# Kernel tuning notes

Hardware: AMD Instinct MI355X
Metric: run time of the kernel (lower is better)

## Reference

```python
import jax, jax.numpy as jnp
import numpy as np

B, S, D, H = 4, 2048, 1024, 16
HD = D // H


def setup_inputs() -> dict:
    key = jax.random.key(0)
    ks = jax.random.split(key, 12)
    s = 1.0 / np.sqrt(D)
    return {
        "query": jax.random.normal(ks[0], (B, S, D), jnp.float32),
        "key_": jax.random.normal(ks[1], (B, S, D), jnp.float32),
        "value": jax.random.normal(ks[2], (B, S, D), jnp.float32),
        "mask": jnp.ones((1, 1, S, S), dtype=bool),
        "Wq": jax.random.normal(ks[3], (D, D), jnp.float32) * s,
        "bq": jnp.zeros((D,), jnp.float32),
        "Wk": jax.random.normal(ks[4], (D, D), jnp.float32) * s,
        "bk": jnp.zeros((D,), jnp.float32),
        "Wv": jax.random.normal(ks[5], (D, D), jnp.float32) * s,
        "bv": jnp.zeros((D,), jnp.float32),
        "Wo": jax.random.normal(ks[6], (D, D), jnp.float32) * s,
        "bo": jnp.zeros((D,), jnp.float32),
    }


def reference(query, key_, value, mask, Wq, bq, Wk, bk, Wv, bv, Wo, bo):
    # Linear projections (torch Linear: x @ W^T + b; here W stored as (in, out))
    Q = query @ Wq + bq   # [B,S,D]
    K = key_ @ Wk + bk
    V = value @ Wv + bv
    # split heads -> [B,H,S,HD]
    Q = Q.reshape(B, S, H, HD).transpose(0, 2, 1, 3)
    K = K.reshape(B, S, H, HD).transpose(0, 2, 1, 3)
    V = V.reshape(B, S, H, HD).transpose(0, 2, 1, 3)
    scores = jnp.einsum("bhqd,bhkd->bhqk", Q, K) / jnp.sqrt(jnp.float32(HD))
    scores = jnp.where(mask, scores, jnp.float32(-jnp.inf))
    attn = jax.nn.softmax(scores, axis=-1)          # [B,H,S,S]
    ctx = jnp.einsum("bhqk,bhkd->bhqd", attn, V)    # dropout = identity (eval)
    ctx = ctx.transpose(0, 2, 1, 3).reshape(B, S, D)
    out = ctx @ Wo + bo
    return out, attn
```

## Files before the change

### kernel.cpp

```cpp
#include <hip/hip_runtime.h>
#include <hip/hip_bf16.h>

typedef __attribute__((ext_vector_type(4))) unsigned short u16x4;
typedef __attribute__((ext_vector_type(8))) short short8;
typedef __attribute__((ext_vector_type(4))) short short4b;
typedef __attribute__((ext_vector_type(4))) float f32x4;

__device__ inline unsigned short f2bf(float f) {
    union { float f; unsigned int i; } v; v.f = f;
    unsigned int r = v.i + 0x7fffu + ((v.i >> 16) & 1u);
    return (unsigned short)(r >> 16);
}

__device__ inline unsigned int pk_bf16(float a, float b) {
    union { __hip_bfloat162 h; unsigned int u; } cv;
    cv.h = __float22bfloat162_rn(float2{a, b});
    return cv.u;
}

#define MFMA_PV(a, b, c) __builtin_amdgcn_mfma_f32_16x16x16bf16_1k((a), (b), (c), 0, 0, 0)
#define MFMA32(a, b, c) __builtin_amdgcn_mfma_f32_16x16x32_bf16((a), (b), (c), 0, 0, 0)

#define SCL 0.18033688011112042f

__device__ inline void gload_lds16(const unsigned short* g, unsigned short* l) {
    __builtin_amdgcn_global_load_lds(
        (const __attribute__((address_space(1))) void*)g,
        (__attribute__((address_space(3))) void*)l,
        16, 0, 0);
}

__global__ __launch_bounds__(256) void convert_f32_bf16(const float* __restrict__ in,
                                                        unsigned short* __restrict__ out,
                                                        int n4) {
    int i = blockIdx.x * 256 + threadIdx.x;
    if (i >= n4) return;
    float4 v = ((const float4*)in)[i];
    u16x4 o = { f2bf(v.x), f2bf(v.y), f2bf(v.z), f2bf(v.w) };
    ((u16x4*)out)[i] = o;
}

__global__ __launch_bounds__(256) void transpose_w(const float* __restrict__ in,
                                                   unsigned short* __restrict__ out) {
    __shared__ unsigned short tile[32][33];
    int c0 = blockIdx.x * 32, r0 = blockIdx.y * 32;
    int x = threadIdx.x & 31, y = threadIdx.x >> 5;
#pragma unroll
    for (int i = 0; i < 4; i++)
        tile[y + i * 8][x] = f2bf(in[(size_t)(r0 + y + i * 8) * 1024 + c0 + x]);
    __syncthreads();
#pragma unroll
    for (int i = 0; i < 4; i++)
        out[(size_t)(c0 + y + i * 8) * 1024 + r0 + x] = tile[x][y + i * 8];
}

template <int F32OUT, int KTILED, int VTILED>
__global__ __launch_bounds__(256) void gemm_bt(const unsigned short* __restrict__ X,
                                               const unsigned short* __restrict__ Wt,
                                               const float* __restrict__ bias,
                                               void* __restrict__ outp,
                                               int M, int N, int K) {
    __shared__ unsigned short As[128 * 64];
    __shared__ unsigned short Bs[128 * 64];
    const int t = threadIdx.x;
    const int l = t & 63, w = t >> 6;
    const int lg = l >> 4, ln = l & 15;
    const int wm = (w >> 1) * 64, wn = (w & 1) * 64;
    const int m0 = blockIdx.y * 128, n0 = blockIdx.x * 128;

    const f32x4 zero = {0.f, 0.f, 0.f, 0.f};
    f32x4 acc[4][4];
#pragma unroll
    for (int i = 0; i < 4; i++)
#pragma unroll
        for (int j = 0; j < 4; j++) acc[i][j] = zero;

    int sr[4], sc[4];
#pragma unroll
    for (int i = 0; i < 4; i++) {
        int pos = i * 2048 + t * 8;
        sr[i] = pos >> 6;
        int c8 = (pos >> 3) & 7;
        sc[i] = (c8 ^ (sr[i] & 7)) * 8;
    }

    for (int k0 = 0; k0 < K; k0 += 64) {
#pragma unroll
        for (int i = 0; i < 4; i++)
            gload_lds16(&X[(size_t)(m0 + sr[i]) * K + k0 + sc[i]], &As[i * 2048 + w * 512]);
#pragma unroll
        for (int i = 0; i < 4; i++)
            gload_lds16(&Wt[(size_t)(n0 + sr[i]) * K + k0 + sc[i]], &Bs[i * 2048 + w * 512]);
        __syncthreads();
#pragma unroll
        for (int kk = 0; kk < 2; kk++) {
            short8 af[4], bfr[4];
#pragma unroll
            for (int i = 0; i < 4; i++) {
                int sl = (((kk << 2) | lg) ^ (ln & 7)) * 8;
                af[i]  = *(const short8*)&As[(wm + i * 16 + ln) * 64 + sl];
                bfr[i] = *(const short8*)&Bs[(wn + i * 16 + ln) * 64 + sl];
            }
#pragma unroll
            for (int i = 0; i < 4; i++)
#pragma unroll
                for (int j = 0; j < 4; j++)
                    acc[i][j] = MFMA32(af[i], bfr[j], acc[i][j]);
        }
        __syncthreads();
    }

#pragma unroll
    for (int j = 0; j < 4; j++) {
        int gn = n0 + wn + j * 16 + ln;
        float bvv = bias[gn];
#pragma unroll
        for (int i = 0; i < 4; i++) {
            int gm = m0 + wm + i * 16 + 4 * lg;
#pragma unroll
            for (int jj = 0; jj < 4; jj++) {
                float val = acc[i][j][jj] + bvv;
                int m = gm + jj, n = gn;
                if (F32OUT) {
                    __builtin_nontemporal_store(val,
                        &((float*)outp)[(size_t)m * N + n]);
                } else if (KTILED) {
                    int b = m >> 11, s = m & 2047;
                    int itk = s >> 5, r = s & 31;
                    int h = n >> 6, dl = n & 63;
                    int cst = (dl >> 3) ^ (r & 7);
                    size_t off = (size_t)(b * 16 + h) * 131072 +
                                 (size_t)itk * 2048 + r * 64 + cst * 8 + (dl & 7);
                    ((unsigned short*)outp)[off] = f2bf(val);
                } else if (VTILED) {
                    int b = m >> 11, s = m & 2047;
                    int h = n >> 6, dl = n & 63;
                    size_t off = (size_t)(b * 16 + h) * 131072 +
                                 (size_t)(s >> 5) * 2048 + ((s >> 4) & 1) * 1024 +
                                 dl * 16 + (s & 15);
                    ((unsigned short*)outp)[off] = f2bf(val);
                } else {
                    ((unsigned short*)outp)[(size_t)m * N + n] = f2bf(val);
                }
            }
        }
    }
}

__global__ __launch_bounds__(256) void attn_fused(const unsigned short* __restrict__ Qp,
                                                  const unsigned short* __restrict__ Kt,
                                                  const unsigned short* __restrict__ Vt,
                                                  float* __restrict__ attn_out,
                                                  unsigned short* __restrict__ Ctx) {
    const int S = 2048, Dm = 1024;
    __shared__ unsigned short Ks[2][4096];
    __shared__ unsigned short Vs[2][4096];

    int blk = blockIdx.x;
    int wid = (blk & 7) * 256 + (blk >> 3);
    int qt = wid & 31, bh = wid >> 5;
    int b = bh >> 4, h = bh & 15;
    int t = threadIdx.x, l = t & 63, w = t >> 6;
    int lg = l >> 4, ln = l & 15;
    int q0 = qt * 64 + w * 16;

    const unsigned short* Qrow = Qp + (size_t)(b * S + q0 + ln) * Dm + h * 64;
    short8 qf0 = *(const short8*)&Qrow[8 * lg];
    short8 qf1 = *(const short8*)&Qrow[32 + 8 * lg];

    const unsigned short* Kb = Kt + (size_t)bh * 131072;
    const unsigned short* Vb = Vt + (size_t)bh * 131072;

    const int c0x = ((0 * 4 + lg) ^ (ln & 7)) * 8;
    const int c1x = ((1 * 4 + lg) ^ (ln & 7)) * 8;
    const int gb0 = 0 * 2048 + 0 * 1024 + ln * 64;
    const int gb1 = 0 * 2048 + 1 * 1024 + ln * 64;
    const int gb2 = 1 * 2048 + 0 * 1024 + ln * 64;
    const int gb3 = 1 * 2048 + 1 * 1024 + ln * 64;

#define STAGE_K64(it, buf) do { \
    gload_lds16(Kb + (size_t)(it) * 4096 + t * 8, &Ks[buf][w * 512]); \
    gload_lds16(Kb + (size_t)(it) * 4096 + 2048 + t * 8, &Ks[buf][2048 + w * 512]); } while (0)
#define STAGE_V64(it, buf) do { \
    gload_lds16(Vb + (size_t)(it) * 4096 + t * 8, &Vs[buf][w * 512]); \
    gload_lds16(Vb + (size_t)(it) * 4096 + 2048 + t * 8, &Vs[buf][2048 + w * 512]); } while (0)

    const f32x4 zero = {0.f, 0.f, 0.f, 0.f};

    float se = 0.f;
    int cur = 0;
    STAGE_K64(0, 0);
    __syncthreads();
    for (int it = 0; it < 32; ++it) {
        if (it < 31) STAGE_K64(it + 1, cur ^ 1);
        f32x4 s[4];
        __builtin_amdgcn_s_setprio(1);
        s[0] = MFMA32(*(const short8*)&Ks[cur][gb0 + c0x], qf0, zero);
        s[0] = MFMA32(*(const short8*)&Ks[cur][gb0 + c1x], qf1, s[0]);
        s[1] = MFMA32(*(const short8*)&Ks[cur][gb1 + c0x], qf0, zero);
        s[1] = MFMA32(*(const short8*)&Ks[cur][gb1 + c1x], qf1, s[1]);
        s[2] = MFMA32(*(const short8*)&Ks[cur][gb2 + c0x], qf0, zero);
        s[2] = MFMA32(*(const short8*)&Ks[cur][gb2 + c1x], qf1, s[2]);
        s[3] = MFMA32(*(const short8*)&Ks[cur][gb3 + c0x], qf0, zero);
        s[3] = MFMA32(*(const short8*)&Ks[cur][gb3 + c1x], qf1, s[3]);
        __builtin_amdgcn_s_setprio(0);
#pragma unroll
        for (int g = 0; g < 4; g++)
            se += exp2f(s[g][0] * SCL) + exp2f(s[g][1] * SCL) +
                  exp2f(s[g][2] * SCL) + exp2f(s[g][3] * SCL);
        __syncthreads();
        cur ^= 1;
    }
    se += __shfl_xor(se, 16);
    se += __shfl_xor(se, 32);
    float nlse = -log2f(se);

    f32x4 acc[4];
#pragma unroll
    for (int i = 0; i < 4; i++) acc[i] = zero;

    float* Arow = attn_out + ((size_t)bh * S + q0 + ln) * S;

    cur = 0;
    STAGE_K64(0, 0);
    STAGE_V64(0, 0);
    __syncthreads();
    for (int it = 0; it < 32; ++it) {
        if (it < 31) { STAGE_K64(it + 1, cur ^ 1); STAGE_V64(it + 1, cur ^ 1); }
        __builtin_amdgcn_sched_barrier(0);
        f32x4 s[4];
        __builtin_amdgcn_s_setprio(1);
        s[0] = MFMA32(*(const short8*)&Ks[cur][gb0 + c0x], qf0, zero);
        s[0] = MFMA32(*(const short8*)&Ks[cur][gb0 + c1x], qf1, s[0]);
        s[1] = MFMA32(*(const short8*)&Ks[cur][gb1 + c0x], qf0, zero);
        s[1] = MFMA32(*(const short8*)&Ks[cur][gb1 + c1x], qf1, s[1]);
        s[2] = MFMA32(*(const short8*)&Ks[cur][gb2 + c0x], qf0, zero);
        s[2] = MFMA32(*(const short8*)&Ks[cur][gb2 + c1x], qf1, s[2]);
        s[3] = MFMA32(*(const short8*)&Ks[cur][gb3 + c0x], qf0, zero);
        s[3] = MFMA32(*(const short8*)&Ks[cur][gb3 + c1x], qf1, s[3]);
        __builtin_amdgcn_s_setprio(0);

        union { short4b v; unsigned int u2[2]; } pf[4];
#pragma unroll
        for (int g = 0; g < 4; g++) {
            f32x4 pw;
#pragma unroll
            for (int j = 0; j < 4; j++)
                pw[j] = exp2f(fmaf(s[g][j], SCL, nlse));
            pf[g].u2[0] = pk_bf16(pw[0], pw[1]);
            pf[g].u2[1] = pk_bf16(pw[2], pw[3]);
            __builtin_nontemporal_store(pw, (f32x4*)&Arow[it * 64 + g * 16 + 4 * lg]);
        }

        __builtin_amdgcn_s_setprio(1);
#pragma unroll
        for (int db = 0; db < 4; db++) {
            int vbase = (db * 16 + ln) * 16 + 4 * lg;
            acc[db] = MFMA_PV(pf[0].v, *(const short4b*)&Vs[cur][0 * 1024 + vbase], acc[db]);
            acc[db] = MFMA_PV(pf[1].v, *(const short4b*)&Vs[cur][1 * 1024 + vbase], acc[db]);
            acc[db] = MFMA_PV(pf[2].v, *(const short4b*)&Vs[cur][2 * 1024 + vbase], acc[db]);
            acc[db] = MFMA_PV(pf[3].v, *(const short4b*)&Vs[cur][3 * 1024 + vbase], acc[db]);
        }
        __builtin_amdgcn_s_setprio(0);
        asm volatile("s_waitcnt vmcnt(4)\n\ts_barrier" ::: "memory");
        cur ^= 1;
    }

#pragma unroll
    for (int db = 0; db < 4; db++)
#pragma unroll
        for (int j = 0; j < 4; j++)
            Ctx[(size_t)(b * S + q0 + 4 * lg + j) * Dm + h * 64 + db * 16 + ln] =
                f2bf(acc[db][j]);
#undef STAGE_K64
#undef STAGE_V64
}

extern "C" void kernel_launch(void* const* d_in, const int* in_sizes, int n_in,
                              void* d_out, int out_size, void* d_ws, size_t ws_size,
                              hipStream_t stream) {
    const float* query = (const float*)d_in[0];
    const float* key_  = (const float*)d_in[1];
    const float* value = (const float*)d_in[2];
    const float* Wq = (const float*)d_in[4];
    const float* bq = (const float*)d_in[5];
    const float* Wk = (const float*)d_in[6];
    const float* bk = (const float*)d_in[7];
    const float* Wv = (const float*)d_in[8];
    const float* bv = (const float*)d_in[9];
    const float* Wo = (const float*)d_in[10];
    const float* bo = (const float*)d_in[11];

    const size_t BSD = (size_t)4 * 2048 * 1024;

    unsigned short* Xbuf = (unsigned short*)d_ws;
    unsigned short* Qp = Xbuf + BSD;
    unsigned short* Kt = Qp + BSD;
    unsigned short* Vt = Kt + BSD;
    unsigned short* WT = Vt + BSD;
    unsigned short* Ctx = Xbuf;

    float* out0 = (float*)d_out;
    float* attn = out0 + BSD;

    dim3 tb(256);
    int n4 = (int)(BSD / 4);
    dim3 cg((n4 + 255) / 256);

    convert_f32_bf16<<<cg, tb, 0, stream>>>(query, Xbuf, n4);
    transpose_w<<<dim3(32, 32), tb, 0, stream>>>(Wq, WT);
    gemm_bt<0, 0, 0><<<dim3(8, 64), tb, 0, stream>>>(Xbuf, WT, bq, Qp, 8192, 1024, 1024);

    convert_f32_bf16<<<cg, tb, 0, stream>>>(key_, Xbuf, n4);
    transpose_w<<<dim3(32, 32), tb, 0, stream>>>(Wk, WT);
    gemm_bt<0, 1, 0><<<dim3(8, 64), tb, 0, stream>>>(Xbuf, WT, bk, Kt, 8192, 1024, 1024);

    convert_f32_bf16<<<cg, tb, 0, stream>>>(value, Xbuf, n4);
    transpose_w<<<dim3(32, 32), tb, 0, stream>>>(Wv, WT);
    gemm_bt<0, 0, 1><<<dim3(8, 64), tb, 0, stream>>>(Xbuf, WT, bv, Vt, 8192, 1024, 1024);

    attn_fused<<<dim3(2048), tb, 0, stream>>>(Qp, Kt, Vt, attn, Ctx);

    transpose_w<<<dim3(32, 32), tb, 0, stream>>>(Wo, WT);
    gemm_bt<1, 0, 0><<<dim3(8, 64), tb, 0, stream>>>(Ctx, WT, bo, out0, 8192, 1024, 1024);
}
```

Measured before the change: 469.8 us.

## Batch conversion and weight-transpose launches; use 128-key tiles in softmax-sum pass

The three input conversions are merged into one launch, and the four weight transposes into one launch with separate workspace buffers. Wo is also transposed a second time later, which is redundant. In the attention kernel, the first pass that computes softmax denominators now stages 128 keys per iteration with a doubled K LDS buffer, halving its loop count and barrier count. The trade-off is more LDS per block, which may lower occupancy, plus extra workspace.

```diff
diff --git a/kernel.cpp b/kernel.cpp
--- a/kernel.cpp
+++ b/kernel.cpp
@@ -30,19 +30,34 @@
         16, 0, 0);
 }
 
-__global__ __launch_bounds__(256) void convert_f32_bf16(const float* __restrict__ in,
-                                                        unsigned short* __restrict__ out,
-                                                        int n4) {
-    int i = blockIdx.x * 256 + threadIdx.x;
-    if (i >= n4) return;
-    float4 v = ((const float4*)in)[i];
-    u16x4 o = { f2bf(v.x), f2bf(v.y), f2bf(v.z), f2bf(v.w) };
+__global__ __launch_bounds__(256) void convert3(const float* __restrict__ q,
+                                                const float* __restrict__ k,
+                                                const float* __restrict__ v,
+                                                unsigned short* __restrict__ Xq,
+                                                unsigned short* __restrict__ Xk,
+                                                unsigned short* __restrict__ Xv) {
+    int bid = blockIdx.x;
+    const float* in = (bid < 8192) ? q : (bid < 16384) ? k : v;
+    unsigned short* out = (bid < 8192) ? Xq : (bid < 16384) ? Xk : Xv;
+    int i = (bid & 8191) * 256 + threadIdx.x;
+    float4 vv = ((const float4*)in)[i];
+    u16x4 o = { f2bf(vv.x), f2bf(vv.y), f2bf(vv.z), f2bf(vv.w) };
     ((u16x4*)out)[i] = o;
 }
 
-__global__ __launch_bounds__(256) void transpose_w(const float* __restrict__ in,
-                                                   unsigned short* __restrict__ out) {
+__global__ __launch_bounds__(256) void transpose_w4(const float* __restrict__ W0,
+                                                    const float* __restrict__ W1,
+                                                    const float* __restrict__ W2,
+                                                    const float* __restrict__ W3,
+                                                    unsigned short* __restrict__ O0,
+                                                    unsigned short* __restrict__ O1,
+                                                    unsigned short* __restrict__ O2,
+                                                    unsigned short* __restrict__ O3) {
     __shared__ unsigned short tile[32][33];
+    const float* in = (blockIdx.z == 0) ? W0 : (blockIdx.z == 1) ? W1
+                    : (blockIdx.z == 2) ? W2 : W3;
+    unsigned short* out = (blockIdx.z == 0) ? O0 : (blockIdx.z == 1) ? O1
+                        : (blockIdx.z == 2) ? O2 : O3;
     int c0 = blockIdx.x * 32, r0 = blockIdx.y * 32;
     int x = threadIdx.x & 31, y = threadIdx.x >> 5;
 #pragma unroll
@@ -153,7 +168,7 @@
                                                   float* __restrict__ attn_out,
                                                   unsigned short* __restrict__ Ctx) {
     const int S = 2048, Dm = 1024;
-    __shared__ unsigned short Ks[2][4096];
+    __shared__ unsigned short Ks[2][8192];
     __shared__ unsigned short Vs[2][4096];
 
     int blk = blockIdx.x;
@@ -173,6 +188,43 @@
 
     const int c0x = ((0 * 4 + lg) ^ (ln & 7)) * 8;
     const int c1x = ((1 * 4 + lg) ^ (ln & 7)) * 8;
+
+    const f32x4 zero = {0.f, 0.f, 0.f, 0.f};
+
+    float se = 0.f;
+    {
+#define STAGE_K128(it, buf) do { \
+    gload_lds16(Kb + (size_t)(it) * 8192 + t * 8, &Ks[buf][w * 512]); \
+    gload_lds16(Kb + (size_t)(it) * 8192 + 2048 + t * 8, &Ks[buf][2048 + w * 512]); \
+    gload_lds16(Kb + (size_t)(it) * 8192 + 4096 + t * 8, &Ks[buf][4096 + w * 512]); \
+    gload_lds16(Kb + (size_t)(it) * 8192 + 6144 + t * 8, &Ks[buf][6144 + w * 512]); } while (0)
+        int cur = 0;
+        STAGE_K128(0, 0);
+        __syncthreads();
+        for (int it = 0; it < 16; ++it) {
+            if (it < 15) STAGE_K128(it + 1, cur ^ 1);
+            f32x4 s[8];
+            __builtin_amdgcn_s_setprio(1);
+#pragma unroll
+            for (int g = 0; g < 8; g++) {
+                int gbase = (g >> 1) * 2048 + (g & 1) * 1024 + ln * 64;
+                s[g] = MFMA32(*(const short8*)&Ks[cur][gbase + c0x], qf0, zero);
+                s[g] = MFMA32(*(const short8*)&Ks[cur][gbase + c1x], qf1, s[g]);
+            }
+            __builtin_amdgcn_s_setprio(0);
+#pragma unroll
+            for (int g = 0; g < 8; g++)
+                se += exp2f(s[g][0] * SCL) + exp2f(s[g][1] * SCL) +
+                      exp2f(s[g][2] * SCL) + exp2f(s[g][3] * SCL);
+            __syncthreads();
+            cur ^= 1;
+        }
+#undef STAGE_K128
+    }
+    se += __shfl_xor(se, 16);
+    se += __shfl_xor(se, 32);
+    float nlse = -log2f(se);
+
     const int gb0 = 0 * 2048 + 0 * 1024 + ln * 64;
     const int gb1 = 0 * 2048 + 1 * 1024 + ln * 64;
     const int gb2 = 1 * 2048 + 0 * 1024 + ln * 64;
@@ -185,43 +237,13 @@
     gload_lds16(Vb + (size_t)(it) * 4096 + t * 8, &Vs[buf][w * 512]); \
     gload_lds16(Vb + (size_t)(it) * 4096 + 2048 + t * 8, &Vs[buf][2048 + w * 512]); } while (0)
 
-    const f32x4 zero = {0.f, 0.f, 0.f, 0.f};
-
-    float se = 0.f;
+    f32x4 acc[4];
+#pragma unroll
+    for (int i = 0; i < 4; i++) acc[i] = zero;
+
+    float* Arow = attn_out + ((size_t)bh * S + q0 + ln) * S;
+
     int cur = 0;
-    STAGE_K64(0, 0);
-    __syncthreads();
-    for (int it = 0; it < 32; ++it) {
-        if (it < 31) STAGE_K64(it + 1, cur ^ 1);
-        f32x4 s[4];
-        __builtin_amdgcn_s_setprio(1);
-        s[0] = MFMA32(*(const short8*)&Ks[cur][gb0 + c0x], qf0, zero);
-        s[0] = MFMA32(*(const short8*)&Ks[cur][gb0 + c1x], qf1, s[0]);
-        s[1] = MFMA32(*(const short8*)&Ks[cur][gb1 + c0x], qf0, zero);
-        s[1] = MFMA32(*(const short8*)&Ks[cur][gb1 + c1x], qf1, s[1]);
-        s[2] = MFMA32(*(const short8*)&Ks[cur][gb2 + c0x], qf0, zero);
-        s[2] = MFMA32(*(const short8*)&Ks[cur][gb2 + c1x], qf1, s[2]);
-        s[3] = MFMA32(*(const short8*)&Ks[cur][gb3 + c0x], qf0, zero);
-        s[3] = MFMA32(*(const short8*)&Ks[cur][gb3 + c1x], qf1, s[3]);
-        __builtin_amdgcn_s_setprio(0);
-#pragma unroll
-        for (int g = 0; g < 4; g++)
-            se += exp2f(s[g][0] * SCL) + exp2f(s[g][1] * SCL) +
-                  exp2f(s[g][2] * SCL) + exp2f(s[g][3] * SCL);
-        __syncthreads();
-        cur ^= 1;
-    }
-    se += __shfl_xor(se, 16);
-    se += __shfl_xor(se, 32);
-    float nlse = -log2f(se);
-
-    f32x4 acc[4];
-#pragma unroll
-    for (int i = 0; i < 4; i++) acc[i] = zero;
-
-    float* Arow = attn_out + ((size_t)bh * S + q0 + ln) * S;
-
-    cur = 0;
     STAGE_K64(0, 0);
     STAGE_V64(0, 0);
     __syncthreads();
@@ -292,35 +314,35 @@
     const float* bo = (const float*)d_in[11];
 
     const size_t BSD = (size_t)4 * 2048 * 1024;
-
-    unsigned short* Xbuf = (unsigned short*)d_ws;
-    unsigned short* Qp = Xbuf + BSD;
-    unsigned short* Kt = Qp + BSD;
-    unsigned short* Vt = Kt + BSD;
-    unsigned short* WT = Vt + BSD;
-    unsigned short* Ctx = Xbuf;
+    const size_t DD  = (size_t)1024 * 1024;
+
+    unsigned short* Xq  = (unsigned short*)d_ws;
+    unsigned short* Xk  = Xq + BSD;
+    unsigned short* Xv  = Xk + BSD;
+    unsigned short* Qp  = Xv + BSD;
+    unsigned short* Kt  = Qp + BSD;
+    unsigned short* Vt  = Kt + BSD;
+    unsigned short* WqT = Vt + BSD;
+    unsigned short* WkT = WqT + DD;
+    unsigned short* WvT = WkT + DD;
+    unsigned short* WoT = WvT + DD;
+    unsigned short* Ctx = Xq;
 
     float* out0 = (float*)d_out;
     float* attn = out0 + BSD;
 
     dim3 tb(256);
-    int n4 = (int)(BSD / 4);
-    dim3 cg((n4 + 255) / 256);
-
-    convert_f32_bf16<<<cg, tb, 0, stream>>>(query, Xbuf, n4);
-    transpose_w<<<dim3(32, 32), tb, 0, stream>>>(Wq, WT);
-    gemm_bt<0, 0, 0><<<dim3(8, 64), tb, 0, stream>>>(Xbuf, WT, bq, Qp, 8192, 1024, 1024);
-
-    convert_f32_bf16<<<cg, tb, 0, stream>>>(key_, Xbuf, n4);
-    transpose_w<<<dim3(32, 32), tb, 0, stream>>>(Wk, WT);
-    gemm_bt<0, 1, 0><<<dim3(8, 64), tb, 0, stream>>>(Xbuf, WT, bk, Kt, 8192, 1024, 1024);
-
-    convert_f32_bf16<<<cg, tb, 0, stream>>>(value, Xbuf, n4);
-    transpose_w<<<dim3(32, 32), tb, 0, stream>>>(Wv, WT);
-    gemm_bt<0, 0, 1><<<dim3(8, 64), tb, 0, stream>>>(Xbuf, WT, bv, Vt, 8192, 1024, 1024);
+
+    convert3<<<dim3(24576), tb, 0, stream>>>(query, key_, value, Xq, Xk, Xv);
+    transpose_w4<<<dim3(32, 32, 4), tb, 0, stream>>>(Wq, Wk, Wv, Wo, WqT, WkT, WvT, WoT);
+
+    gemm_bt<0, 0, 0><<<dim3(8, 64), tb, 0, stream>>>(Xq, WqT, bq, Qp, 8192, 1024, 1024);
+    gemm_bt<0, 1, 0><<<dim3(8, 64), tb, 0, stream>>>(Xk, WkT, bk, Kt, 8192, 1024, 1024);
+    gemm_bt<0, 0, 1><<<dim3(8, 64), tb, 0, stream>>>(Xv, WvT, bv, Vt, 8192, 1024, 1024);
 
     attn_fused<<<dim3(2048), tb, 0, stream>>>(Qp, Kt, Vt, attn, Ctx);
 
-    transpose_w<<<dim3(32, 32), tb, 0, stream>>>(Wo, WT);
-    gemm_bt<1, 0, 0><<<dim3(8, 64), tb, 0, stream>>>(Ctx, WT, bo, out0, 8192, 1024, 1024);
-}
+    transpose_w4<<<dim3(32, 32, 1), tb, 0, stream>>>(Wo, Wo, Wo, Wo, WoT, WoT, WoT, WoT);
+
+    gemm_bt<1, 0, 0><<<dim3(8, 64), tb, 0, stream>>>(Ctx, WoT, bo, out0, 8192, 1024, 1024);
+}
```

New measurement: 461.1 us. About the same (-1.9%).
